# Performance work log

Hardware: AMD Instinct MI355X
Metric: run time of the kernel (lower is better)

## Reference

```python
import jax, jax.numpy as jnp
import numpy as np

N_EMBD = 1024
N_HEAD = 16
B, T = 4, 2048

def setup_inputs() -> dict:
    key = jax.random.key(0)
    k1, k2, k3 = jax.random.split(key, 3)
    scale = 0.02
    return {
        "x": jax.random.normal(k1, (B, T, N_EMBD), dtype=jnp.float32),
        "W_qkv": jax.random.normal(k2, (N_EMBD, 3 * N_EMBD), dtype=jnp.float32) * scale,
        "b_qkv": jnp.zeros((3 * N_EMBD,), dtype=jnp.float32),
        "W_proj": jax.random.normal(k3, (N_EMBD, N_EMBD), dtype=jnp.float32) * scale,
        "b_proj": jnp.zeros((N_EMBD,), dtype=jnp.float32),
    }

def reference(x, W_qkv, b_qkv, W_proj, b_proj):
    Bb, Tt, C = x.shape
    hs = C // N_HEAD  # head_size
    qkv = x @ W_qkv + b_qkv                      # [B,T,3C]
    q, k, v = jnp.split(qkv, 3, axis=-1)
    # [B,T,C] -> [B,H,T,hs]
    def to_heads(t):
        return t.reshape(Bb, Tt, N_HEAD, hs).transpose(0, 2, 1, 3)
    q, k, v = to_heads(q), to_heads(k), to_heads(v)
    scores = jnp.einsum('bhqd,bhkd->bhqk', q, k) * (1.0 / np.sqrt(hs))
    causal = jnp.tril(jnp.ones((Tt, Tt), dtype=bool))
    scores = jnp.where(causal, scores, -jnp.inf)
    weights = jax.nn.softmax(scores, axis=-1)    # dropout=0.0 -> identity
    out = jnp.einsum('bhqk,bhkd->bhqd', weights, v)
    out = out.transpose(0, 2, 1, 3).reshape(Bb, Tt, C)
    return out @ W_proj + b_proj
```

## Files before the change

### kernel.cpp

```cpp
#include <hip/hip_runtime.h>
#include <cstdint>

typedef _Float16 f16;
typedef _Float16 f16x4 __attribute__((ext_vector_type(4)));
typedef _Float16 f16x8 __attribute__((ext_vector_type(8)));
typedef float f32x4 __attribute__((ext_vector_type(4)));

constexpr int NB = 4, NT = 2048, NC = 1024, NH = 16, HS = 64;
constexpr int Mtot = NB * NT;
constexpr int BM = 128, BN = 128;

__device__ __forceinline__ void gll16(const f16* g, f16* l) {
  __builtin_amdgcn_global_load_lds(
      (const __attribute__((address_space(1))) unsigned int*)(uintptr_t)g,
      (__attribute__((address_space(3))) unsigned int*)(uintptr_t)l, 16, 0, 0);
}

__global__ __launch_bounds__(256) void convert_x(
    const float* __restrict__ X, f16* __restrict__ Xh)
{
  const size_t i = ((size_t)blockIdx.x * 256 + threadIdx.x) * 8;
  float4 a = *reinterpret_cast<const float4*>(X + i);
  float4 b = *reinterpret_cast<const float4*>(X + i + 4);
  f16x8 o;
  o[0] = (f16)a.x; o[1] = (f16)a.y; o[2] = (f16)a.z; o[3] = (f16)a.w;
  o[4] = (f16)b.x; o[5] = (f16)b.y; o[6] = (f16)b.z; o[7] = (f16)b.w;
  *reinterpret_cast<f16x8*>(Xh + i) = o;
}

__global__ __launch_bounds__(256) void transpose_w(
    const float* __restrict__ Wq, const float* __restrict__ Wp,
    f16* __restrict__ Wqt, f16* __restrict__ Wpt)
{
  __shared__ __align__(16) f16 Ts[64 * 72];
  const int bx = blockIdx.x;
  const float* src; f16* dst; int Ndim, n0;
  if (bx < 48) { src = Wq; dst = Wqt; Ndim = 3 * NC; n0 = bx * 64; }
  else         { src = Wp; dst = Wpt; Ndim = NC;     n0 = (bx - 48) * 64; }
  const int k0 = blockIdx.y * 64;
  const int t = threadIdx.x;
  const int kl = t >> 2, nb = (t & 3) * 16;
#pragma unroll
  for (int i = 0; i < 4; ++i) {
    float4 vv = *reinterpret_cast<const float4*>(
        src + (size_t)(k0 + kl) * Ndim + n0 + nb + 4 * i);
    f16x4 h; h[0] = (f16)vv.x; h[1] = (f16)vv.y; h[2] = (f16)vv.z; h[3] = (f16)vv.w;
    *reinterpret_cast<f16x4*>(&Ts[kl * 72 + nb + 4 * i]) = h;
  }
  __syncthreads();
  const int nl = t >> 2, kb = (t & 3) * 16;
#pragma unroll
  for (int i = 0; i < 2; ++i) {
    f16x8 o;
#pragma unroll
    for (int j = 0; j < 8; ++j) o[j] = Ts[(kb + 8 * i + j) * 72 + nl];
    *reinterpret_cast<f16x8*>(dst + (size_t)(n0 + nl) * NC + k0 + kb + 8 * i) = o;
  }
}

template <int MODE>
__global__ __launch_bounds__(256) void gemm_f16(
    const f16* __restrict__ A, const f16* __restrict__ Bt,
    const float* __restrict__ bias,
    f16* __restrict__ Qh, f16* __restrict__ Kh, f16* __restrict__ Vh,
    float* __restrict__ Out, int ntiles)
{
  __shared__ __align__(16) f16 As[BM * 64];
  __shared__ __align__(16) f16 Bs[BN * 64];
  const int tid = threadIdx.x;
  const int flat = blockIdx.x;
  const int cpx = gridDim.x >> 3;
  const int v = (flat & 7) * cpx + (flat >> 3);
  const int m0 = (v / ntiles) * BM;
  const int n0 = (v % ntiles) * BN;
  const int w = tid >> 6, l = tid & 63;
  const int wr = w >> 1, wc = w & 1;
  const int lr = l & 15, hi = l >> 4;

  f32x4 acc[4][4];
#pragma unroll
  for (int i = 0; i < 4; ++i)
#pragma unroll
    for (int j = 0; j < 4; ++j) acc[i][j] = (f32x4){0.f, 0.f, 0.f, 0.f};

  const int lrow = l >> 3;
  const int lsrc = ((l & 7) ^ lrow) * 8;

  for (int k0 = 0; k0 < NC; k0 += 64) {
    __syncthreads();
#pragma unroll
    for (int i = 0; i < 4; ++i) {
      const int rr = 32 * w + 8 * i;
      gll16(A  + (size_t)(m0 + rr + lrow) * NC + k0 + lsrc, &As[rr * 64]);
      gll16(Bt + (size_t)(n0 + rr + lrow) * NC + k0 + lsrc, &Bs[rr * 64]);
    }
    __syncthreads();
#pragma unroll
    for (int kk = 0; kk < 2; ++kk) {
      f16x8 a[4], b[4];
#pragma unroll
      for (int mi = 0; mi < 4; ++mi) {
        int row = wr * 64 + mi * 16 + lr;
        int idx = (row * 64 + kk * 32 + hi * 8) ^ ((row & 7) << 3);
        a[mi] = *reinterpret_cast<const f16x8*>(&As[idx]);
      }
#pragma unroll
      for (int ni = 0; ni < 4; ++ni) {
        int row = wc * 64 + ni * 16 + lr;
        int idx = (row * 64 + kk * 32 + hi * 8) ^ ((row & 7) << 3);
        b[ni] = *reinterpret_cast<const f16x8*>(&Bs[idx]);
      }
#pragma unroll
      for (int mi = 0; mi < 4; ++mi)
#pragma unroll
        for (int ni = 0; ni < 4; ++ni)
          acc[mi][ni] = __builtin_amdgcn_mfma_f32_16x16x32_f16(
              a[mi], b[ni], acc[mi][ni], 0, 0, 0);
    }
  }

  if (MODE == 0) {
#pragma unroll
    for (int ni = 0; ni < 4; ++ni) {
      int colg = n0 + wc * 64 + ni * 16 + lr;
      int which = colg >> 10;
      int c = colg & (NC - 1);
      int h = c >> 6, d = c & 63;
      f16* dst = (which == 0) ? Qh : ((which == 1) ? Kh : Vh);
      float bv = bias[colg];
#pragma unroll
      for (int mi = 0; mi < 4; ++mi) {
#pragma unroll
        for (int r = 0; r < 4; ++r) {
          int rowg = m0 + wr * 64 + mi * 16 + hi * 4 + r;
          int b = rowg >> 11, t = rowg & (NT - 1);
          dst[(((size_t)(b * NH + h) * NT) + t) * HS + d] =
              (f16)(acc[mi][ni][r] + bv);
        }
      }
    }
  } else {
#pragma unroll
    for (int ni = 0; ni < 4; ++ni) {
      int colg = n0 + wc * 64 + ni * 16 + lr;
      float bv = bias[colg];
#pragma unroll
      for (int mi = 0; mi < 4; ++mi) {
#pragma unroll
        for (int r = 0; r < 4; ++r) {
          int rowg = m0 + wr * 64 + mi * 16 + hi * 4 + r;
          Out[(size_t)rowg * NC + colg] = acc[mi][ni][r] + bv;
        }
      }
    }
  }
}

__global__ __launch_bounds__(128, 2) void flash_attn(
    const f16* __restrict__ Qh, const f16* __restrict__ Kh,
    const f16* __restrict__ Vh, f16* __restrict__ att)
{
  __shared__ __align__(16) f16 Ks[2][64 * 64];
  __shared__ __align__(16) f16 Vt[2][64 * 64];

  const int tid = threadIdx.x;
  const int w = tid >> 6, l = tid & 63;
  const int lr = l & 15, g = l >> 4;

  const int flat = blockIdx.x;
  const int v = (flat & 7) * 128 + (flat >> 3);
  const int pairi = v & 15;
  const int bh = v >> 4;

  const f16* Qb = Qh + (size_t)bh * NT * HS;
  const f16* Kb = Kh + (size_t)bh * NT * HS;
  const f16* Vb = Vh + (size_t)bh * NT * HS;
  const int ob = bh >> 4, oh = bh & (NH - 1);

  const int srow = tid >> 1;
  const int scol = (tid & 1) * 32;
  const int ksl = ((srow >> 5) & 1) * 32 + ((srow >> 2) & 3) * 8 +
                  ((srow >> 4) & 1) * 4 + (srow & 3);

  f16x8 kpre[4], vpre[4];
#pragma unroll
  for (int ii = 0; ii < 4; ++ii) {
    kpre[ii] = *reinterpret_cast<const f16x8*>(Kb + (size_t)srow * HS + scol + 8 * ii);
    vpre[ii] = *reinterpret_cast<const f16x8*>(Vb + (size_t)srow * HS + scol + 8 * ii);
  }

  for (int seg = 0; seg < 2; ++seg) {
    const int qt = (seg == 0) ? pairi : 31 - pairi;
    const int qbase = qt * 64 + w * 32;
    const int jtmax = qt;

    f16x8 qB[2][2];
#pragma unroll
    for (int mt = 0; mt < 2; ++mt)
#pragma unroll
      for (int ds = 0; ds < 2; ++ds) {
        f16x8 t = *reinterpret_cast<const f16x8*>(
            Qb + (size_t)(qbase + 16 * mt + lr) * HS + 32 * ds + 8 * g);
#pragma unroll
        for (int j = 0; j < 8; ++j) t[j] = t[j] * (f16)0.18033688f;
        qB[mt][ds] = t;
      }

    f32x4 Ot[2][4];
    float m_run[2], l_run[2];
#pragma unroll
    for (int mt = 0; mt < 2; ++mt) {
#pragma unroll
      for (int dt = 0; dt < 4; ++dt) Ot[mt][dt] = (f32x4){0.f, 0.f, 0.f, 0.f};
      m_run[mt] = -INFINITY; l_run[mt] = 0.f;
    }

    for (int jt = 0; jt <= jtmax; ++jt) {
      const int cur = jt & 1;
#pragma unroll
      for (int ii = 0; ii < 4; ++ii) {
        int c0 = scol + 8 * ii;
        *reinterpret_cast<f16x8*>(&Ks[cur][srow * 64 + (c0 ^ ((srow & 7) << 3))]) = kpre[ii];
#pragma unroll
        for (int j = 0; j < 8; ++j) {
          int d = c0 + j;
          int s = (d + (d >> 3)) & 7;
          Vt[cur][d * 64 + (ksl ^ (s << 3))] = vpre[ii][j];
        }
      }
      const bool more = (jt < jtmax) || (seg == 0);
      if (more) {
        const int nj = (jt < jtmax) ? jt + 1 : 0;
#pragma unroll
        for (int ii = 0; ii < 4; ++ii) {
          kpre[ii] = *reinterpret_cast<const f16x8*>(
              Kb + (size_t)(nj * 64 + srow) * HS + scol + 8 * ii);
          vpre[ii] = *reinterpret_cast<const f16x8*>(
              Vb + (size_t)(nj * 64 + srow) * HS + scol + 8 * ii);
        }
      }
      __syncthreads();

      if (jt * 64 > qbase + 31) continue;

      const bool needMask = (jt * 64 + 63) > qbase;

      f16x8 aK[4][2];
#pragma unroll
      for (int kt2 = 0; kt2 < 4; ++kt2) {
        int row = 16 * kt2 + lr;
#pragma unroll
        for (int ds = 0; ds < 2; ++ds)
          aK[kt2][ds] = *reinterpret_cast<const f16x8*>(
              &Ks[cur][row * 64 + ((32 * ds + 8 * g) ^ ((row & 7) << 3))]);
      }

      f16x8 pB[2][2];

#pragma unroll
      for (int mt = 0; mt < 2; ++mt) {
        f32x4 St[4];
#pragma unroll
        for (int kt2 = 0; kt2 < 4; ++kt2) St[kt2] = (f32x4){0.f, 0.f, 0.f, 0.f};
        __builtin_amdgcn_s_setprio(1);
#pragma unroll
        for (int kt2 = 0; kt2 < 4; ++kt2)
#pragma unroll
          for (int ds = 0; ds < 2; ++ds)
            St[kt2] = __builtin_amdgcn_mfma_f32_16x16x32_f16(
                aK[kt2][ds], qB[mt][ds], St[kt2], 0, 0, 0);
        __builtin_amdgcn_s_setprio(0);

        const int qg = qbase + 16 * mt + lr;
        if (needMask) {
#pragma unroll
          for (int kt2 = 0; kt2 < 4; ++kt2)
#pragma unroll
            for (int r = 0; r < 4; ++r)
              if ((jt * 64 + 16 * kt2 + 4 * g + r) > qg) St[kt2][r] = -INFINITY;
        }
        float pm = -INFINITY;
#pragma unroll
        for (int kt2 = 0; kt2 < 4; ++kt2)
#pragma unroll
          for (int r = 0; r < 4; ++r) pm = fmaxf(pm, St[kt2][r]);
        pm = fmaxf(pm, __shfl_xor(pm, 16));
        pm = fmaxf(pm, __shfl_xor(pm, 32));
        float mo = m_run[mt];
        if (!__all(pm <= mo + 8.0f)) {
          float mn = fmaxf(mo, pm);
          float al = exp2f(mo - mn);
          l_run[mt] *= al;
#pragma unroll
          for (int dt = 0; dt < 4; ++dt)
#pragma unroll
            for (int r = 0; r < 4; ++r) Ot[mt][dt][r] *= al;
          m_run[mt] = mn;
          mo = mn;
        }
        float ts = 0.f;
#pragma unroll
        for (int kt2 = 0; kt2 < 4; ++kt2) {
#pragma unroll
          for (int r = 0; r < 4; ++r) {
            float pp = exp2f(St[kt2][r] - mo);
            ts += pp;
            pB[mt][kt2 >> 1][(kt2 & 1) * 4 + r] = (f16)pp;
          }
        }
        ts += __shfl_xor(ts, 16);
        ts += __shfl_xor(ts, 32);
        l_run[mt] += ts;
      }

      __builtin_amdgcn_s_setprio(1);
#pragma unroll
      for (int kt = 0; kt < 2; ++kt)
#pragma unroll
        for (int dt = 0; dt < 4; ++dt) {
          int d = 16 * dt + lr;
          int s = (d + (d >> 3)) & 7;
          f16x8 vA = *reinterpret_cast<const f16x8*>(
              &Vt[cur][d * 64 + ((32 * kt + 8 * g) ^ (s << 3))]);
#pragma unroll
          for (int mt = 0; mt < 2; ++mt)
            Ot[mt][dt] = __builtin_amdgcn_mfma_f32_16x16x32_f16(
                vA, pB[mt][kt], Ot[mt][dt], 0, 0, 0);
        }
      __builtin_amdgcn_s_setprio(0);
    }

    __syncthreads();
    f16* scr = &Ks[0][0] + w * 2048;
#pragma unroll
    for (int mt = 0; mt < 2; ++mt) {
      float inv = 1.f / l_run[mt];
      int q = 16 * mt + lr;
#pragma unroll
      for (int dt = 0; dt < 4; ++dt) {
        f16x4 ok;
#pragma unroll
        for (int r = 0; r < 4; ++r) ok[r] = (f16)(Ot[mt][dt][r] * inv);
        *reinterpret_cast<f16x4*>(
            &scr[q * 64 + ((16 * dt + 4 * g) ^ ((q & 7) << 3))]) = ok;
      }
    }
    const int orow = l >> 1;
    const int ocol = (l & 1) * 32;
#pragma unroll
    for (int i = 0; i < 4; ++i) {
      f16x8 ov = *reinterpret_cast<const f16x8*>(
          &scr[orow * 64 + ((ocol + i * 8) ^ ((orow & 7) << 3))]);
      *reinterpret_cast<f16x8*>(
          &att[((size_t)(ob * NT + qbase + orow)) * NC + oh * HS + ocol + i * 8]) = ov;
    }
    __syncthreads();
  }
}

extern "C" void kernel_launch(void* const* d_in, const int* in_sizes, int n_in,
                              void* d_out, int out_size, void* d_ws, size_t ws_size,
                              hipStream_t stream)
{
  (void)in_sizes; (void)n_in; (void)out_size; (void)ws_size;
  const float* x     = (const float*)d_in[0];
  const float* Wqkv  = (const float*)d_in[1];
  const float* bqkv  = (const float*)d_in[2];
  const float* Wproj = (const float*)d_in[3];
  const float* bproj = (const float*)d_in[4];
  float* out = (float*)d_out;

  const size_t HE = (size_t)NB * NH * NT * HS;
  f16* Qh  = (f16*)d_ws;
  f16* Kh  = Qh + HE;
  f16* Vh  = Kh + HE;
  f16* XA  = Vh + HE;
  f16* Wqt = XA + HE;
  f16* Wpt = Wqt + (size_t)3 * NC * NC;

  convert_x<<<dim3(Mtot * NC / (256 * 8)), 256, 0, stream>>>(x, XA);
  transpose_w<<<dim3(64, 16), 256, 0, stream>>>(Wqkv, Wproj, Wqt, Wpt);
  gemm_f16<0><<<dim3(64 * 24), 256, 0, stream>>>(XA, Wqt, bqkv, Qh, Kh, Vh, nullptr, 24);
  flash_attn<<<dim3(1024), 128, 0, stream>>>(Qh, Kh, Vh, XA);
  gemm_f16<1><<<dim3(64 * 8), 256, 0, stream>>>(XA, Wpt, bproj, nullptr, nullptr, nullptr, out, 8);
}
```

Measured before the change: 192.6 us.

## Split paired causal q-tiles into separate heaviest-first blocks with single-buffered LDS

The flash attention kernel no longer has each block process a pair of q-tiles (light plus heavy) for load balance. It now launches one block per q-tile, 2048 blocks in total, ordered so the heaviest tiles are scheduled first. The K/V LDS buffers drop from double to single buffering, which halves shared memory. Launch bounds are raised to 4 blocks per SM to increase occupancy. The cost is a second barrier per key tile, since the buffer must be drained before it is overwritten, and less in-block overlap of LDS writes with compute.

```diff
diff --git a/kernel.cpp b/kernel.cpp
--- a/kernel.cpp
+++ b/kernel.cpp
@@ -156,27 +156,30 @@
   }
 }
 
-__global__ __launch_bounds__(128, 2) void flash_attn(
+__global__ __launch_bounds__(128, 4) void flash_attn(
     const f16* __restrict__ Qh, const f16* __restrict__ Kh,
     const f16* __restrict__ Vh, f16* __restrict__ att)
 {
-  __shared__ __align__(16) f16 Ks[2][64 * 64];
-  __shared__ __align__(16) f16 Vt[2][64 * 64];
+  __shared__ __align__(16) f16 Ks[64 * 64];
+  __shared__ __align__(16) f16 Vt[64 * 64];
 
   const int tid = threadIdx.x;
   const int w = tid >> 6, l = tid & 63;
   const int lr = l & 15, g = l >> 4;
 
   const int flat = blockIdx.x;
-  const int v = (flat & 7) * 128 + (flat >> 3);
-  const int pairi = v & 15;
-  const int bh = v >> 4;
+  const int v = (flat & 7) * 256 + (flat >> 3);
+  const int qt = 31 - (v & 31);
+  const int bh = v >> 5;
 
   const f16* Qb = Qh + (size_t)bh * NT * HS;
   const f16* Kb = Kh + (size_t)bh * NT * HS;
   const f16* Vb = Vh + (size_t)bh * NT * HS;
   const int ob = bh >> 4, oh = bh & (NH - 1);
 
+  const int qbase = qt * 64 + w * 32;
+  const int jtmax = qt;
+
   const int srow = tid >> 1;
   const int scol = (tid & 1) * 32;
   const int ksl = ((srow >> 5) & 1) * 32 + ((srow >> 2) & 3) * 8 +
@@ -189,60 +192,51 @@
     vpre[ii] = *reinterpret_cast<const f16x8*>(Vb + (size_t)srow * HS + scol + 8 * ii);
   }
 
-  for (int seg = 0; seg < 2; ++seg) {
-    const int qt = (seg == 0) ? pairi : 31 - pairi;
-    const int qbase = qt * 64 + w * 32;
-    const int jtmax = qt;
-
-    f16x8 qB[2][2];
-#pragma unroll
-    for (int mt = 0; mt < 2; ++mt)
-#pragma unroll
-      for (int ds = 0; ds < 2; ++ds) {
-        f16x8 t = *reinterpret_cast<const f16x8*>(
-            Qb + (size_t)(qbase + 16 * mt + lr) * HS + 32 * ds + 8 * g);
-#pragma unroll
-        for (int j = 0; j < 8; ++j) t[j] = t[j] * (f16)0.18033688f;
-        qB[mt][ds] = t;
-      }
-
-    f32x4 Ot[2][4];
-    float m_run[2], l_run[2];
-#pragma unroll
-    for (int mt = 0; mt < 2; ++mt) {
-#pragma unroll
-      for (int dt = 0; dt < 4; ++dt) Ot[mt][dt] = (f32x4){0.f, 0.f, 0.f, 0.f};
-      m_run[mt] = -INFINITY; l_run[mt] = 0.f;
-    }
-
-    for (int jt = 0; jt <= jtmax; ++jt) {
-      const int cur = jt & 1;
+  f16x8 qB[2][2];
+#pragma unroll
+  for (int mt = 0; mt < 2; ++mt)
+#pragma unroll
+    for (int ds = 0; ds < 2; ++ds) {
+      f16x8 t = *reinterpret_cast<const f16x8*>(
+          Qb + (size_t)(qbase + 16 * mt + lr) * HS + 32 * ds + 8 * g);
+#pragma unroll
+      for (int j = 0; j < 8; ++j) t[j] = t[j] * (f16)0.18033688f;
+      qB[mt][ds] = t;
+    }
+
+  f32x4 Ot[2][4];
+  float m_run[2], l_run[2];
+#pragma unroll
+  for (int mt = 0; mt < 2; ++mt) {
+#pragma unroll
+    for (int dt = 0; dt < 4; ++dt) Ot[mt][dt] = (f32x4){0.f, 0.f, 0.f, 0.f};
+    m_run[mt] = -INFINITY; l_run[mt] = 0.f;
+  }
+
+  for (int jt = 0; jt <= jtmax; ++jt) {
+#pragma unroll
+    for (int ii = 0; ii < 4; ++ii) {
+      int c0 = scol + 8 * ii;
+      *reinterpret_cast<f16x8*>(&Ks[srow * 64 + (c0 ^ ((srow & 7) << 3))]) = kpre[ii];
+#pragma unroll
+      for (int j = 0; j < 8; ++j) {
+        int d = c0 + j;
+        int s = (d + (d >> 3)) & 7;
+        Vt[d * 64 + (ksl ^ (s << 3))] = vpre[ii][j];
+      }
+    }
+    if (jt < jtmax) {
 #pragma unroll
       for (int ii = 0; ii < 4; ++ii) {
-        int c0 = scol + 8 * ii;
-        *reinterpret_cast<f16x8*>(&Ks[cur][srow * 64 + (c0 ^ ((srow & 7) << 3))]) = kpre[ii];
-#pragma unroll
-        for (int j = 0; j < 8; ++j) {
-          int d = c0 + j;
-          int s = (d + (d >> 3)) & 7;
-          Vt[cur][d * 64 + (ksl ^ (s << 3))] = vpre[ii][j];
-        }
-      }
-      const bool more = (jt < jtmax) || (seg == 0);
-      if (more) {
-        const int nj = (jt < jtmax) ? jt + 1 : 0;
-#pragma unroll
-        for (int ii = 0; ii < 4; ++ii) {
-          kpre[ii] = *reinterpret_cast<const f16x8*>(
-              Kb + (size_t)(nj * 64 + srow) * HS + scol + 8 * ii);
-          vpre[ii] = *reinterpret_cast<const f16x8*>(
-              Vb + (size_t)(nj * 64 + srow) * HS + scol + 8 * ii);
-        }
-      }
-      __syncthreads();
-
-      if (jt * 64 > qbase + 31) continue;
-
+        kpre[ii] = *reinterpret_cast<const f16x8*>(
+            Kb + (size_t)((jt + 1) * 64 + srow) * HS + scol + 8 * ii);
+        vpre[ii] = *reinterpret_cast<const f16x8*>(
+            Vb + (size_t)((jt + 1) * 64 + srow) * HS + scol + 8 * ii);
+      }
+    }
+    __syncthreads();
+
+    {
       const bool needMask = (jt * 64 + 63) > qbase;
 
       f16x8 aK[4][2];
@@ -252,7 +246,7 @@
 #pragma unroll
         for (int ds = 0; ds < 2; ++ds)
           aK[kt2][ds] = *reinterpret_cast<const f16x8*>(
-              &Ks[cur][row * 64 + ((32 * ds + 8 * g) ^ ((row & 7) << 3))]);
+              &Ks[row * 64 + ((32 * ds + 8 * g) ^ ((row & 7) << 3))]);
       }
 
       f16x8 pB[2][2];
@@ -321,7 +315,7 @@
           int d = 16 * dt + lr;
           int s = (d + (d >> 3)) & 7;
           f16x8 vA = *reinterpret_cast<const f16x8*>(
-              &Vt[cur][d * 64 + ((32 * kt + 8 * g) ^ (s << 3))]);
+              &Vt[d * 64 + ((32 * kt + 8 * g) ^ (s << 3))]);
 #pragma unroll
           for (int mt = 0; mt < 2; ++mt)
             Ot[mt][dt] = __builtin_amdgcn_mfma_f32_16x16x32_f16(
@@ -329,32 +323,31 @@
         }
       __builtin_amdgcn_s_setprio(0);
     }
-
     __syncthreads();
-    f16* scr = &Ks[0][0] + w * 2048;
-#pragma unroll
-    for (int mt = 0; mt < 2; ++mt) {
-      float inv = 1.f / l_run[mt];
-      int q = 16 * mt + lr;
-#pragma unroll
-      for (int dt = 0; dt < 4; ++dt) {
-        f16x4 ok;
-#pragma unroll
-        for (int r = 0; r < 4; ++r) ok[r] = (f16)(Ot[mt][dt][r] * inv);
-        *reinterpret_cast<f16x4*>(
-            &scr[q * 64 + ((16 * dt + 4 * g) ^ ((q & 7) << 3))]) = ok;
-      }
-    }
-    const int orow = l >> 1;
-    const int ocol = (l & 1) * 32;
-#pragma unroll
-    for (int i = 0; i < 4; ++i) {
-      f16x8 ov = *reinterpret_cast<const f16x8*>(
-          &scr[orow * 64 + ((ocol + i * 8) ^ ((orow & 7) << 3))]);
-      *reinterpret_cast<f16x8*>(
-          &att[((size_t)(ob * NT + qbase + orow)) * NC + oh * HS + ocol + i * 8]) = ov;
-    }
-    __syncthreads();
+  }
+
+  f16* scr = &Ks[0] + w * 2048;
+#pragma unroll
+  for (int mt = 0; mt < 2; ++mt) {
+    float inv = 1.f / l_run[mt];
+    int q = 16 * mt + lr;
+#pragma unroll
+    for (int dt = 0; dt < 4; ++dt) {
+      f16x4 ok;
+#pragma unroll
+      for (int r = 0; r < 4; ++r) ok[r] = (f16)(Ot[mt][dt][r] * inv);
+      *reinterpret_cast<f16x4*>(
+          &scr[q * 64 + ((16 * dt + 4 * g) ^ ((q & 7) << 3))]) = ok;
+    }
+  }
+  const int orow = l >> 1;
+  const int ocol = (l & 1) * 32;
+#pragma unroll
+  for (int i = 0; i < 4; ++i) {
+    f16x8 ov = *reinterpret_cast<const f16x8*>(
+        &scr[orow * 64 + ((ocol + i * 8) ^ ((orow & 7) << 3))]);
+    *reinterpret_cast<f16x8*>(
+        &att[((size_t)(ob * NT + qbase + orow)) * NC + oh * HS + ocol + i * 8]) = ov;
   }
 }
 
@@ -381,6 +374,6 @@
   convert_x<<<dim3(Mtot * NC / (256 * 8)), 256, 0, stream>>>(x, XA);
   transpose_w<<<dim3(64, 16), 256, 0, stream>>>(Wqkv, Wproj, Wqt, Wpt);
   gemm_f16<0><<<dim3(64 * 24), 256, 0, stream>>>(XA, Wqt, bqkv, Qh, Kh, Vh, nullptr, 24);
-  flash_attn<<<dim3(1024), 128, 0, stream>>>(Qh, Kh, Vh, XA);
+  flash_attn<<<dim3(2048), 128, 0, stream>>>(Qh, Kh, Vh, XA);
   gemm_f16<1><<<dim3(64 * 8), 256, 0, stream>>>(XA, Wpt, bproj, nullptr, nullptr, nullptr, out, 8);
 }
```

Result: slower. 515.2 us (+167.5%).
